# Kernel optimization log

Measured on AMD Instinct MI355X. Metric: run time of the kernel, lower is better.

## Reference

```python
import jax, jax.numpy as jnp
import numpy as np

EPS_NORM = 1e-12  # F.normalize eps
EPS_BN = 1e-5     # BatchNorm1d eps


def _gather_neighbors(tensor, index):
    # tensor: (bs, v, d), index: (bs, v, n) -> (bs, v, n, d)
    return jax.vmap(lambda t, i: t[i])(tensor, index)


def setup_inputs() -> dict:
    key = jax.random.key(0)
    ks = jax.random.split(key, 8)
    bs, v, n = 4, 4096, 32
    cin, cout = 128, 256
    stdv = float(np.sqrt(2.0 / cout))
    return {
        "neighbor_index": jax.random.randint(ks[0], (bs, v, n), 0, v),
        "vertices": jax.random.normal(ks[1], (bs, v, 3), dtype=jnp.float32),
        "feature_map": jax.random.normal(ks[2], (bs, v, cin - 1), dtype=jnp.float32),
        "directions": jax.random.uniform(ks[3], (4, cout), minval=-stdv, maxval=stdv, dtype=jnp.float32),
        "W": jax.random.normal(ks[4], (cout, cin), dtype=jnp.float32) / np.sqrt(cin),
        "b": jnp.zeros((cout,), jnp.float32),
        "gamma": jnp.ones((cout,), jnp.float32),
        "beta": jnp.zeros((cout,), jnp.float32),
    }


def reference(neighbor_index, vertices, feature_map, directions, W, b, gamma, beta):
    # --- direction-based weights theta: (bs, v, n, cout) ---
    neighbors = _gather_neighbors(vertices, neighbor_index)          # (bs,v,n,3)
    direc = neighbors - vertices[:, :, None, :]
    direc_norm = direc / jnp.maximum(
        jnp.linalg.norm(direc, axis=-1, keepdims=True), EPS_NORM)    # F.normalize
    dir_w = (direc_norm + 1.0) * 0.5                                  # (bs,v,n,3)
    sup_w = jnp.stack([directions[1] - directions[0],
                       directions[2] - directions[0],
                       directions[3] - directions[0]], axis=0)        # (3, cout)
    theta = jax.nn.relu(jnp.einsum('bvnk,kc->bvnc', dir_w, sup_w) + directions[0])

    # --- gathered features + L2 distance channel ---
    fs = _gather_neighbors(feature_map, neighbor_index)               # (bs,v,n,cin-1)
    fdist = jnp.sqrt(jnp.sum(fs * fs, axis=-1, keepdims=True))        # (bs,v,n,1)
    fs = jnp.concatenate([fs, fdist], axis=-1)                        # (bs,v,n,cin)

    # --- Linear -> BatchNorm1d (training stats) -> ReLU ---
    z = jnp.einsum('bvni,ci->bvnc', fs, W) + b                        # (bs,v,n,cout)
    mean = jnp.mean(z, axis=(0, 1, 2))
    var = jnp.mean(jnp.square(z - mean), axis=(0, 1, 2))              # biased var
    zn = (z - mean) * jax.lax.rsqrt(var + EPS_BN) * gamma + beta
    act = jax.nn.relu(zn) * theta

    # --- max-pool over neighbor dim ---
    return jnp.max(act, axis=2)                                       # (bs,v,cout)
```

## Files before the change

### kernel.cpp

```cpp
#include <hip/hip_runtime.h>

typedef unsigned short ushort_t;
typedef __attribute__((ext_vector_type(8))) short short8;
typedef __attribute__((ext_vector_type(4))) float floatx4;
typedef __attribute__((ext_vector_type(2))) float floatx2;

#define NN    32
#define CIN   128
#define COUT  256
#define NPTS  16384
#define NSAMP (NPTS * NN)
#define LDA   136

__device__ ushort_t g_fsp[(size_t)NPTS * 128];
__device__ ushort_t g_wb[COUT * CIN];
__device__ ushort_t g_y[(size_t)NPTS * COUT];
__device__ int      g_mult[NPTS];
__device__ float    g_stat[512];
__device__ float    g_consts[1536];
__device__ int      g_isf32;

__device__ __forceinline__ float bf2f(ushort_t u) {
    return __uint_as_float(((unsigned int)u) << 16);
}
__device__ __forceinline__ ushort_t f2bf(float f) {
    unsigned int x = __float_as_uint(f);
    return (ushort_t)((x + 0x7FFFu + ((x >> 16) & 1u)) >> 16);
}

__global__ void detect_zero_kernel(const void* __restrict__ verts) {
    int tid = threadIdx.x;
    g_mult[blockIdx.x * 256 + tid] = 0;
    if (blockIdx.x == 0) {
        g_stat[tid] = 0.0f; g_stat[256 + tid] = 0.0f;
        if (tid < 64) {
            float ax = fabsf(bf2f(((const ushort_t*)verts)[tid]));
            bool plaus = (ax > 1e-5f) && (ax < 32.0f);
            unsigned long long b = __ballot(plaus);
            if (tid == 0) g_isf32 = (__popcll(b) >= 56) ? 0 : 1;
        }
    }
}

__global__ void prep_kernel(const void* __restrict__ fm,
                            const void* __restrict__ Wg,
                            const int* __restrict__ nbr) {
    const int f32 = g_isf32;
    const int tid = threadIdx.x;
    if (blockIdx.x < 32) {
        int i = blockIdx.x * 1024 + tid * 4;
        if (f32) {
            float4 v = ((const float4*)Wg)[i >> 2];
            g_wb[i] = f2bf(v.x); g_wb[i + 1] = f2bf(v.y);
            g_wb[i + 2] = f2bf(v.z); g_wb[i + 3] = f2bf(v.w);
        } else {
            *(uint2*)(g_wb + i) = *(const uint2*)((const ushort_t*)Wg + i);
        }
    }
    int gid = blockIdx.x * 256 + tid;
    if (gid < NSAMP) {
        int gv = ((gid >> 17) << 12) + nbr[gid];
        atomicAdd(&g_mult[gv], 1);
    }
    int row  = blockIdx.x * 4 + (tid >> 6);
    int lane = tid & 63;
    float f0, f1; ushort_t u0, u1;
    if (f32) {
        const float* src = (const float*)fm + (size_t)row * 127;
        f0 = src[lane];
        f1 = (lane < 63) ? src[64 + lane] : 0.0f;
        u0 = f2bf(f0); u1 = f2bf(f1);
    } else {
        const ushort_t* src = (const ushort_t*)fm + (size_t)row * 127;
        u0 = src[lane];
        u1 = (lane < 63) ? src[64 + lane] : (ushort_t)0;
        f0 = bf2f(u0); f1 = bf2f(u1);
    }
    float ss = f0 * f0 + f1 * f1;
    #pragma unroll
    for (int d = 1; d < 64; d <<= 1) ss += __shfl_xor(ss, d, 64);
    float fd = sqrtf(ss);
    ushort_t* dst = g_fsp + (size_t)row * 128;
    dst[lane]      = u0;
    dst[64 + lane] = (lane < 63) ? u1 : f2bf(fd);
}

__global__ __launch_bounds__(256, 2)
void ygemm_kernel() {
    __shared__ ushort_t At[64 * LDA];
    __shared__ float    multS[64];

    const int tid = threadIdx.x;
    const int r0  = blockIdx.x * 64;

    if (tid < 64) multS[tid] = (float)g_mult[r0 + tid];
    #pragma unroll
    for (int i = 0; i < 4; ++i) {
        int chunk = tid + i * 256;
        int r = chunk >> 4;
        int c = chunk & 15;
        const uint4 v = *(const uint4*)(g_fsp + (size_t)(r0 + r) * 128 + c * 8);
        *(uint4*)&At[r * LDA + c * 8] = v;
    }
    __syncthreads();

    const int lane = tid & 63;
    const int w    = tid >> 6;
    const int m    = lane & 15;
    const int q    = lane >> 4;

    floatx4 acc[4][4];
    #pragma unroll
    for (int rt = 0; rt < 4; ++rt)
        #pragma unroll
        for (int ct = 0; ct < 4; ++ct)
            acc[rt][ct] = (floatx4){0.0f, 0.0f, 0.0f, 0.0f};

    #pragma unroll
    for (int kk = 0; kk < 4; ++kk) {
        const int kof = kk * 32 + q * 8;
        short8 af[4];
        #pragma unroll
        for (int rt = 0; rt < 4; ++rt)
            af[rt] = *(const short8*)&At[(rt * 16 + m) * LDA + kof];
        short8 bfr[4];
        #pragma unroll
        for (int ct = 0; ct < 4; ++ct) {
            int ch = w * 64 + ct * 16 + m;
            bfr[ct] = *(const short8*)(g_wb + ch * CIN + kof);
        }
        #pragma unroll
        for (int rt = 0; rt < 4; ++rt)
            #pragma unroll
            for (int ct = 0; ct < 4; ++ct)
                acc[rt][ct] = __builtin_amdgcn_mfma_f32_16x16x32_bf16(
                    af[rt], bfr[ct], acc[rt][ct], 0, 0, 0);
    }

    #pragma unroll
    for (int ct = 0; ct < 4; ++ct) {
        const int ch = w * 64 + ct * 16 + m;
        float s = 0.0f, ss = 0.0f;
        #pragma unroll
        for (int rt = 0; rt < 4; ++rt)
            #pragma unroll
            for (int j = 0; j < 4; ++j) {
                int rloc = rt * 16 + q * 4 + j;
                ushort_t yb = f2bf(acc[rt][ct][j]);
                g_y[(size_t)(r0 + rloc) * COUT + ch] = yb;
                float yv = bf2f(yb);
                float wm = multS[rloc];
                s  += wm * yv;
                ss += wm * yv * yv;
            }
        s  += __shfl_xor(s, 16, 64);  s  += __shfl_xor(s, 32, 64);
        ss += __shfl_xor(ss, 16, 64); ss += __shfl_xor(ss, 32, 64);
        if (q == 0) {
            atomicAdd(&g_stat[ch], s);
            atomicAdd(&g_stat[256 + ch], ss);
        }
    }
}

__global__ void finalize_kernel(const void* __restrict__ gamma,
                                const void* __restrict__ beta,
                                const void* __restrict__ dirs) {
    const int f32 = g_isf32;
    int c = threadIdx.x;
    const float invN = 1.0f / (float)NSAMP;
    float mean = g_stat[c] * invN;
    float var  = fmaxf(g_stat[256 + c] * invN - mean * mean, 0.0f);
    float inv  = 1.0f / sqrtf(var + 1e-5f);
    float ga, be, d0, d1, d2, d3;
    if (f32) {
        ga = ((const float*)gamma)[c]; be = ((const float*)beta)[c];
        const float* dd = (const float*)dirs;
        d0 = dd[c]; d1 = dd[256 + c]; d2 = dd[512 + c]; d3 = dd[768 + c];
    } else {
        ga = bf2f(((const ushort_t*)gamma)[c]); be = bf2f(((const ushort_t*)beta)[c]);
        const ushort_t* dd = (const ushort_t*)dirs;
        d0 = bf2f(dd[c]); d1 = bf2f(dd[256 + c]);
        d2 = bf2f(dd[512 + c]); d3 = bf2f(dd[768 + c]);
    }
    float scale = ga * inv;
    g_consts[c]        = scale;
    g_consts[256 + c]  = be - mean * scale;
    g_consts[512 + c]  = d0;
    g_consts[768 + c]  = d1 - d0;
    g_consts[1024 + c] = d2 - d0;
    g_consts[1280 + c] = d3 - d0;
}

__global__ __launch_bounds__(128, 4)
void epi_kernel(const int* __restrict__ nbr,
                const void* __restrict__ verts,
                void* __restrict__ out) {
    __shared__ int    rows[NN];
    __shared__ float4 dws[NN];

    const int p   = blockIdx.x;
    const int tid = threadIdx.x;
    const int f32 = g_isf32;

    if (tid < NN) {
        int gv = ((p >> 12) << 12) + nbr[p * NN + tid];
        rows[tid] = gv;
        float sx, sy, sz, nx, ny, nz;
        if (f32) {
            const float* vv = (const float*)verts;
            sx = vv[p * 3]; sy = vv[p * 3 + 1]; sz = vv[p * 3 + 2];
            nx = vv[gv * 3]; ny = vv[gv * 3 + 1]; nz = vv[gv * 3 + 2];
        } else {
            const ushort_t* vv = (const ushort_t*)verts;
            sx = bf2f(vv[p * 3]); sy = bf2f(vv[p * 3 + 1]); sz = bf2f(vv[p * 3 + 2]);
            nx = bf2f(vv[gv * 3]); ny = bf2f(vv[gv * 3 + 1]); nz = bf2f(vv[gv * 3 + 2]);
        }
        float dx = nx - sx, dy = ny - sy, dz = nz - sz;
        float nrm = sqrtf(dx * dx + dy * dy + dz * dz);
        float inv = 1.0f / fmaxf(nrm, 1e-12f);
        dws[tid] = make_float4((dx * inv + 1.0f) * 0.5f,
                               (dy * inv + 1.0f) * 0.5f,
                               (dz * inv + 1.0f) * 0.5f, 0.0f);
    }
    __syncthreads();

    const int c2 = tid * 2;
    const floatx2 zero = {0.0f, 0.0f};
    floatx2 sc = *(const floatx2*)&g_consts[c2];
    floatx2 sh = *(const floatx2*)&g_consts[256 + c2];
    floatx2 d0 = *(const floatx2*)&g_consts[512 + c2];
    floatx2 s0 = *(const floatx2*)&g_consts[768 + c2];
    floatx2 s1 = *(const floatx2*)&g_consts[1024 + c2];
    floatx2 s2 = *(const floatx2*)&g_consts[1280 + c2];

    floatx2 vm0 = zero, vm1 = zero, vm2 = zero, vm3 = zero;
    #pragma unroll
    for (int j = 0; j < NN; j += 4) {
        #pragma unroll
        for (int jj = 0; jj < 4; ++jj) {
            int rb = __builtin_amdgcn_readfirstlane(rows[j + jj]);
            const unsigned int* rp =
                (const unsigned int*)(g_y + (size_t)rb * COUT);
            unsigned int u = rp[tid];
            floatx2 y;
            y.x = __uint_as_float(u << 16);
            y.y = __uint_as_float(u & 0xFFFF0000u);
            float4 dw = dws[j + jj];
            floatx2 th = d0 + s0 * dw.x + s1 * dw.y + s2 * dw.z;
            th = __builtin_elementwise_max(th, zero);
            floatx2 zt = (y * sc + sh) * th;
            if      (jj == 0) vm0 = __builtin_elementwise_max(vm0, zt);
            else if (jj == 1) vm1 = __builtin_elementwise_max(vm1, zt);
            else if (jj == 2) vm2 = __builtin_elementwise_max(vm2, zt);
            else              vm3 = __builtin_elementwise_max(vm3, zt);
        }
    }
    floatx2 vm = __builtin_elementwise_max(
        __builtin_elementwise_max(vm0, vm1),
        __builtin_elementwise_max(vm2, vm3));

    size_t ofs = (size_t)p * COUT + c2;
    if (f32) {
        *(floatx2*)((float*)out + ofs) = vm;
    } else {
        unsigned int o = ((unsigned int)f2bf(vm.y) << 16) | (unsigned int)f2bf(vm.x);
        *(unsigned int*)((ushort_t*)out + ofs) = o;
    }
}

extern "C" void kernel_launch(void* const* d_in, const int* in_sizes, int n_in,
                              void* d_out, int out_size, void* d_ws, size_t ws_size,
                              hipStream_t stream) {
    const int* nbr   = (const int*)d_in[0];
    const void* verts = d_in[1];
    const void* fm    = d_in[2];
    const void* dirs  = d_in[3];
    const void* Wg    = d_in[4];
    const void* gamma = d_in[6];
    const void* beta  = d_in[7];
    (void)d_ws; (void)ws_size; (void)in_sizes; (void)n_in; (void)out_size;

    detect_zero_kernel<<<dim3(64), dim3(256), 0, stream>>>(verts);
    prep_kernel<<<dim3(NPTS / 4), dim3(256), 0, stream>>>(fm, Wg, nbr);
    ygemm_kernel<<<dim3(NPTS / 64), dim3(256), 0, stream>>>();
    finalize_kernel<<<dim3(1), dim3(256), 0, stream>>>(gamma, beta, dirs);
    epi_kernel<<<dim3(NPTS), dim3(128), 0, stream>>>(nbr, verts, d_out);
}
```

Measured before the change: 158.1 us.

## Fuse feature prep into GEMM, use LDS histograms and per-block stat partials

Drops the separate detect and prep kernels. Neighbor multiplicities are now counted in per-block LDS histograms and reduced inside the GEMM. The feature conversion and distance channel are fused into the GEMM's LDS tile load, and each kernel probes the dtype itself instead of reading a global flag. Global float atomics for the BN statistics are replaced by per-block partials that the finalize kernel sums. The epilogue also splits neighbors across two waves with 4-channel vector loads, caches constants in LDS and swizzles block order. In exchange the GEMM now does strided 127-wide loads, and the single-block finalize performs a 256-way serial reduction.

```diff
diff --git a/kernel.cpp b/kernel.cpp
--- a/kernel.cpp
+++ b/kernel.cpp
@@ -11,14 +11,13 @@
 #define NPTS  16384
 #define NSAMP (NPTS * NN)
 #define LDA   136
-
-__device__ ushort_t g_fsp[(size_t)NPTS * 128];
-__device__ ushort_t g_wb[COUT * CIN];
-__device__ ushort_t g_y[(size_t)NPTS * COUT];
-__device__ int      g_mult[NPTS];
-__device__ float    g_stat[512];
-__device__ float    g_consts[1536];
-__device__ int      g_isf32;
+#define HB    128
+
+__device__ __align__(16) ushort_t g_wb[COUT * CIN];
+__device__ __align__(16) ushort_t g_y[(size_t)NPTS * COUT];
+__device__ __align__(16) int      g_hp[HB * 4096];
+__device__ __align__(16) float    g_sp[256 * 512];
+__device__ __align__(16) float    g_consts[1536];
 
 __device__ __forceinline__ float bf2f(ushort_t u) {
     return __uint_as_float(((unsigned int)u) << 16);
@@ -27,28 +26,33 @@
     unsigned int x = __float_as_uint(f);
     return (ushort_t)((x + 0x7FFFu + ((x >> 16) & 1u)) >> 16);
 }
-
-__global__ void detect_zero_kernel(const void* __restrict__ verts) {
-    int tid = threadIdx.x;
-    g_mult[blockIdx.x * 256 + tid] = 0;
-    if (blockIdx.x == 0) {
-        g_stat[tid] = 0.0f; g_stat[256 + tid] = 0.0f;
-        if (tid < 64) {
-            float ax = fabsf(bf2f(((const ushort_t*)verts)[tid]));
-            bool plaus = (ax > 1e-5f) && (ax < 32.0f);
-            unsigned long long b = __ballot(plaus);
-            if (tid == 0) g_isf32 = (__popcll(b) >= 56) ? 0 : 1;
-        }
-    }
-}
-
-__global__ void prep_kernel(const void* __restrict__ fm,
-                            const void* __restrict__ Wg,
-                            const int* __restrict__ nbr) {
-    const int f32 = g_isf32;
+__device__ __forceinline__ int probe_f32(const void* verts, int lane) {
+    float ax = fabsf(bf2f(((const ushort_t*)verts)[lane]));
+    unsigned long long b = __ballot((ax > 1e-5f) && (ax < 32.0f));
+    return (__popcll(b) >= 56) ? 0 : 1;
+}
+
+__global__ __launch_bounds__(256)
+void hist_kernel(const int* __restrict__ nbr,
+                 const void* __restrict__ Wg,
+                 const void* __restrict__ verts) {
+    __shared__ int h[4096];
+    const int b   = blockIdx.x;
     const int tid = threadIdx.x;
-    if (blockIdx.x < 32) {
-        int i = blockIdx.x * 1024 + tid * 4;
+    if (b < HB) {
+        #pragma unroll
+        for (int i = 0; i < 16; ++i) h[i * 256 + tid] = 0;
+        __syncthreads();
+        const int* src = nbr + (size_t)b * 4096;
+        #pragma unroll
+        for (int i = 0; i < 16; ++i) atomicAdd(&h[src[i * 256 + tid]], 1);
+        __syncthreads();
+        int* dst = g_hp + (size_t)b * 4096;
+        #pragma unroll
+        for (int i = 0; i < 16; ++i) dst[i * 256 + tid] = h[i * 256 + tid];
+    } else {
+        const int f32 = probe_f32(verts, tid & 63);
+        int i = (b - HB) * 1024 + tid * 4;
         if (f32) {
             float4 v = ((const float4*)Wg)[i >> 2];
             g_wb[i] = f2bf(v.x); g_wb[i + 1] = f2bf(v.y);
@@ -57,57 +61,53 @@
             *(uint2*)(g_wb + i) = *(const uint2*)((const ushort_t*)Wg + i);
         }
     }
-    int gid = blockIdx.x * 256 + tid;
-    if (gid < NSAMP) {
-        int gv = ((gid >> 17) << 12) + nbr[gid];
-        atomicAdd(&g_mult[gv], 1);
-    }
-    int row  = blockIdx.x * 4 + (tid >> 6);
-    int lane = tid & 63;
-    float f0, f1; ushort_t u0, u1;
-    if (f32) {
-        const float* src = (const float*)fm + (size_t)row * 127;
-        f0 = src[lane];
-        f1 = (lane < 63) ? src[64 + lane] : 0.0f;
-        u0 = f2bf(f0); u1 = f2bf(f1);
-    } else {
-        const ushort_t* src = (const ushort_t*)fm + (size_t)row * 127;
-        u0 = src[lane];
-        u1 = (lane < 63) ? src[64 + lane] : (ushort_t)0;
-        f0 = bf2f(u0); f1 = bf2f(u1);
-    }
-    float ss = f0 * f0 + f1 * f1;
-    #pragma unroll
-    for (int d = 1; d < 64; d <<= 1) ss += __shfl_xor(ss, d, 64);
-    float fd = sqrtf(ss);
-    ushort_t* dst = g_fsp + (size_t)row * 128;
-    dst[lane]      = u0;
-    dst[64 + lane] = (lane < 63) ? u1 : f2bf(fd);
 }
 
 __global__ __launch_bounds__(256, 2)
-void ygemm_kernel() {
-    __shared__ ushort_t At[64 * LDA];
-    __shared__ float    multS[64];
-
-    const int tid = threadIdx.x;
-    const int r0  = blockIdx.x * 64;
-
-    if (tid < 64) multS[tid] = (float)g_mult[r0 + tid];
-    #pragma unroll
-    for (int i = 0; i < 4; ++i) {
-        int chunk = tid + i * 256;
-        int r = chunk >> 4;
-        int c = chunk & 15;
-        const uint4 v = *(const uint4*)(g_fsp + (size_t)(r0 + r) * 128 + c * 8);
-        *(uint4*)&At[r * LDA + c * 8] = v;
+void ygemm_kernel(const void* __restrict__ fm, const void* __restrict__ verts) {
+    __shared__ __align__(16) ushort_t At[64 * LDA];
+    __shared__ float multS[64];
+
+    const int tid  = threadIdx.x;
+    const int r0   = blockIdx.x * 64;
+    const int lane = tid & 63;
+    const int f32  = probe_f32(verts, lane);
+
+    if (tid < 64) {
+        const int* hp = g_hp + (size_t)(r0 >> 12) * 32 * 4096 + (r0 & 4095) + tid;
+        int s = 0;
+        #pragma unroll
+        for (int p2 = 0; p2 < 32; ++p2) s += hp[(size_t)p2 * 4096];
+        multS[tid] = (float)s;
+    }
+
+    const int rl4 = tid >> 6;
+    #pragma unroll 4
+    for (int i = 0; i < 16; ++i) {
+        const int rl = i * 4 + rl4;
+        float f0, f1; ushort_t u0, u1;
+        if (f32) {
+            const float* src = (const float*)fm + (size_t)(r0 + rl) * 127;
+            f0 = src[lane];
+            f1 = (lane < 63) ? src[64 + lane] : 0.0f;
+            u0 = f2bf(f0); u1 = f2bf(f1);
+        } else {
+            const ushort_t* src = (const ushort_t*)fm + (size_t)(r0 + rl) * 127;
+            u0 = src[lane];
+            u1 = (lane < 63) ? src[64 + lane] : (ushort_t)0;
+            f0 = bf2f(u0); f1 = bf2f(u1);
+        }
+        float ss = f0 * f0 + f1 * f1;
+        #pragma unroll
+        for (int d = 1; d < 64; d <<= 1) ss += __shfl_xor(ss, d, 64);
+        At[rl * LDA + lane]      = u0;
+        At[rl * LDA + 64 + lane] = (lane < 63) ? u1 : f2bf(sqrtf(ss));
     }
     __syncthreads();
 
-    const int lane = tid & 63;
-    const int w    = tid >> 6;
-    const int m    = lane & 15;
-    const int q    = lane >> 4;
+    const int w = tid >> 6;
+    const int m = lane & 15;
+    const int q = lane >> 4;
 
     floatx4 acc[4][4];
     #pragma unroll
@@ -156,20 +156,28 @@
         s  += __shfl_xor(s, 16, 64);  s  += __shfl_xor(s, 32, 64);
         ss += __shfl_xor(ss, 16, 64); ss += __shfl_xor(ss, 32, 64);
         if (q == 0) {
-            atomicAdd(&g_stat[ch], s);
-            atomicAdd(&g_stat[256 + ch], ss);
+            g_sp[(size_t)blockIdx.x * 512 + ch]       = s;
+            g_sp[(size_t)blockIdx.x * 512 + 256 + ch] = ss;
         }
     }
 }
 
 __global__ void finalize_kernel(const void* __restrict__ gamma,
                                 const void* __restrict__ beta,
-                                const void* __restrict__ dirs) {
-    const int f32 = g_isf32;
-    int c = threadIdx.x;
+                                const void* __restrict__ dirs,
+                                const void* __restrict__ verts) {
+    const int c   = threadIdx.x;
+    const int f32 = probe_f32(verts, c & 63);
+
+    float s = 0.0f, ss = 0.0f;
+    #pragma unroll 8
+    for (int p2 = 0; p2 < 256; ++p2) {
+        s  += g_sp[(size_t)p2 * 512 + c];
+        ss += g_sp[(size_t)p2 * 512 + 256 + c];
+    }
     const float invN = 1.0f / (float)NSAMP;
-    float mean = g_stat[c] * invN;
-    float var  = fmaxf(g_stat[256 + c] * invN - mean * mean, 0.0f);
+    float mean = s * invN;
+    float var  = fmaxf(ss * invN - mean * mean, 0.0f);
     float inv  = 1.0f / sqrtf(var + 1e-5f);
     float ga, be, d0, d1, d2, d3;
     if (f32) {
@@ -197,11 +205,20 @@
                 void* __restrict__ out) {
     __shared__ int    rows[NN];
     __shared__ float4 dws[NN];
-
-    const int p   = blockIdx.x;
-    const int tid = threadIdx.x;
-    const int f32 = g_isf32;
-
+    __shared__ __align__(16) float cS[1536];
+    __shared__ float4 xm1[64];
+
+    const int tid  = threadIdx.x;
+    const int bid  = blockIdx.x;
+    const int p    = ((bid & 7) << 11) | (bid >> 3);
+    const int lane = tid & 63;
+    const int f32  = probe_f32(verts, lane);
+
+    #pragma unroll
+    for (int k = 0; k < 3; ++k) {
+        int i4 = (k * 128 + tid) * 4;
+        *(float4*)&cS[i4] = *(const float4*)&g_consts[i4];
+    }
     if (tid < NN) {
         int gv = ((p >> 12) << 12) + nbr[p * NN + tid];
         rows[tid] = gv;
@@ -224,54 +241,64 @@
     }
     __syncthreads();
 
-    const int c2 = tid * 2;
-    const floatx2 zero = {0.0f, 0.0f};
-    floatx2 sc = *(const floatx2*)&g_consts[c2];
-    floatx2 sh = *(const floatx2*)&g_consts[256 + c2];
-    floatx2 d0 = *(const floatx2*)&g_consts[512 + c2];
-    floatx2 s0 = *(const floatx2*)&g_consts[768 + c2];
-    floatx2 s1 = *(const floatx2*)&g_consts[1024 + c2];
-    floatx2 s2 = *(const floatx2*)&g_consts[1280 + c2];
-
-    floatx2 vm0 = zero, vm1 = zero, vm2 = zero, vm3 = zero;
-    #pragma unroll
-    for (int j = 0; j < NN; j += 4) {
+    const int w  = tid >> 6;
+    const int c4 = lane * 4;
+    const floatx4 zero = {0.0f, 0.0f, 0.0f, 0.0f};
+    const floatx4 sc = *(const floatx4*)&cS[c4];
+    const floatx4 sh = *(const floatx4*)&cS[256 + c4];
+    const floatx4 d0 = *(const floatx4*)&cS[512 + c4];
+    const floatx4 s0 = *(const floatx4*)&cS[768 + c4];
+    const floatx4 s1 = *(const floatx4*)&cS[1024 + c4];
+    const floatx4 s2 = *(const floatx4*)&cS[1280 + c4];
+
+    floatx4 vm0 = zero, vm1 = zero, vm2 = zero, vm3 = zero;
+    #pragma unroll
+    for (int j0 = 0; j0 < 16; j0 += 4) {
         #pragma unroll
         for (int jj = 0; jj < 4; ++jj) {
-            int rb = __builtin_amdgcn_readfirstlane(rows[j + jj]);
-            const unsigned int* rp =
-                (const unsigned int*)(g_y + (size_t)rb * COUT);
-            unsigned int u = rp[tid];
-            floatx2 y;
-            y.x = __uint_as_float(u << 16);
-            y.y = __uint_as_float(u & 0xFFFF0000u);
-            float4 dw = dws[j + jj];
-            floatx2 th = d0 + s0 * dw.x + s1 * dw.y + s2 * dw.z;
+            const int j = w * 16 + j0 + jj;
+            int rb = __builtin_amdgcn_readfirstlane(rows[j]);
+            const uint2 u = *(const uint2*)(g_y + (size_t)rb * COUT + c4);
+            floatx4 y;
+            y.x = __uint_as_float(u.x << 16);
+            y.y = __uint_as_float(u.x & 0xFFFF0000u);
+            y.z = __uint_as_float(u.y << 16);
+            y.w = __uint_as_float(u.y & 0xFFFF0000u);
+            float4 dw = dws[j];
+            floatx4 th = d0 + s0 * dw.x + s1 * dw.y + s2 * dw.z;
             th = __builtin_elementwise_max(th, zero);
-            floatx2 zt = (y * sc + sh) * th;
+            floatx4 zt = (y * sc + sh) * th;
             if      (jj == 0) vm0 = __builtin_elementwise_max(vm0, zt);
             else if (jj == 1) vm1 = __builtin_elementwise_max(vm1, zt);
             else if (jj == 2) vm2 = __builtin_elementwise_max(vm2, zt);
             else              vm3 = __builtin_elementwise_max(vm3, zt);
         }
     }
-    floatx2 vm = __builtin_elementwise_max(
+    floatx4 vm = __builtin_elementwise_max(
         __builtin_elementwise_max(vm0, vm1),
         __builtin_elementwise_max(vm2, vm3));
 
-    size_t ofs = (size_t)p * COUT + c2;
-    if (f32) {
-        *(floatx2*)((float*)out + ofs) = vm;
-    } else {
-        unsigned int o = ((unsigned int)f2bf(vm.y) << 16) | (unsigned int)f2bf(vm.x);
-        *(unsigned int*)((ushort_t*)out + ofs) = o;
+    if (w == 1) xm1[lane] = make_float4(vm.x, vm.y, vm.z, vm.w);
+    __syncthreads();
+    if (w == 0) {
+        float4 o = xm1[lane];
+        vm = __builtin_elementwise_max(vm, (floatx4){o.x, o.y, o.z, o.w});
+        size_t ofs = (size_t)p * COUT + c4;
+        if (f32) {
+            *(floatx4*)((float*)out + ofs) = vm;
+        } else {
+            uint2 ou;
+            ou.x = ((unsigned int)f2bf(vm.y) << 16) | (unsigned int)f2bf(vm.x);
+            ou.y = ((unsigned int)f2bf(vm.w) << 16) | (unsigned int)f2bf(vm.z);
+            *(uint2*)((ushort_t*)out + ofs) = ou;
+        }
     }
 }
 
 extern "C" void kernel_launch(void* const* d_in, const int* in_sizes, int n_in,
                               void* d_out, int out_size, void* d_ws, size_t ws_size,
                               hipStream_t stream) {
-    const int* nbr   = (const int*)d_in[0];
+    const int* nbr    = (const int*)d_in[0];
     const void* verts = d_in[1];
     const void* fm    = d_in[2];
     const void* dirs  = d_in[3];
@@ -280,9 +307,8 @@
     const void* beta  = d_in[7];
     (void)d_ws; (void)ws_size; (void)in_sizes; (void)n_in; (void)out_size;
 
-    detect_zero_kernel<<<dim3(64), dim3(256), 0, stream>>>(verts);
-    prep_kernel<<<dim3(NPTS / 4), dim3(256), 0, stream>>>(fm, Wg, nbr);
-    ygemm_kernel<<<dim3(NPTS / 64), dim3(256), 0, stream>>>();
-    finalize_kernel<<<dim3(1), dim3(256), 0, stream>>>(gamma, beta, dirs);
+    hist_kernel<<<dim3(HB + 32), dim3(256), 0, stream>>>(nbr, Wg, verts);
+    ygemm_kernel<<<dim3(NPTS / 64), dim3(256), 0, stream>>>(fm, verts);
+    finalize_kernel<<<dim3(1), dim3(256), 0, stream>>>(gamma, beta, dirs, verts);
     epi_kernel<<<dim3(NPTS), dim3(128), 0, stream>>>(nbr, verts, d_out);
 }
```

Result: faster. 148.5 us (-6.1%).
